# Kernel optimization log

Measured on AMD Instinct MI355X. Metric: run time of the kernel, lower is better.

The kernel has to match this reference:

```python
import jax, jax.numpy as jnp
import numpy as np

B, C, N = 8, 256, 2048

def setup_inputs() -> dict:
    key = jax.random.key(0)
    ks = jax.random.split(key, 7)
    s = 1.0 / np.sqrt(C)
    return {
        "x": jax.random.normal(ks[0], (B, C, N), dtype=jnp.float32),
        "Wq": jax.random.normal(ks[1], (C, C), dtype=jnp.float32) * s,
        "bq": jax.random.normal(ks[2], (C,), dtype=jnp.float32) * s,
        "Wk": jax.random.normal(ks[3], (C, C), dtype=jnp.float32) * s,
        "bk": jax.random.normal(ks[4], (C,), dtype=jnp.float32) * s,
        "Wv": jax.random.normal(ks[5], (C, C), dtype=jnp.float32) * s,
        "bv": jax.random.normal(ks[6], (C,), dtype=jnp.float32) * s,
    }

def reference(x, Wq, bq, Wk, bk, Wv, bv):
    # x: [B, C, N]; Conv1d(k=1) == channel-mixing matmul + bias
    q = jnp.einsum('oc,bcn->bon', Wq, x) + bq[None, :, None]  # [B,C,N]
    k = jnp.einsum('oc,bcn->bon', Wk, x) + bk[None, :, None]  # [B,C,N]
    v = jnp.einsum('oc,bcn->bon', Wv, x) + bv[None, :, None]  # [B,C,N]
    # qk = bmm(q^T, k): [B, N, N]
    qk = jnp.einsum('bcn,bcm->bnm', q, k)
    # global-sum normalization over the ENTIRE qk tensor (not row-wise softmax)
    attn_w = qk / jnp.sum(qk)
    # attn = bmm(v, attn_w): [B, C, N]
    attn = jnp.einsum('bcn,bnm->bcm', v, attn_w)
    return attn
```

## Files before the change

### kernel.cpp

```cpp
#include <hip/hip_runtime.h>


typedef _Float16 half8 __attribute__((ext_vector_type(8)));
typedef _Float16 half4 __attribute__((ext_vector_type(4)));
typedef _Float16 half2v __attribute__((ext_vector_type(2)));
typedef float f4v __attribute__((ext_vector_type(4)));

#define GP  40
#define GPB 36

__launch_bounds__(256)
__global__ void k1_kernel(const float* __restrict__ x, const float* __restrict__ Wq,
                          const float* __restrict__ Wk, const float* __restrict__ bq,
                          const float* __restrict__ bk, float* __restrict__ sxpart,
                          float* __restrict__ W3, float* __restrict__ u2,
                          float* __restrict__ w1, float* __restrict__ s1,
                          float* __restrict__ S, float* __restrict__ Gpart) {
    __shared__ __align__(16) char smem[40960];
    const int blk = blockIdx.x, t = threadIdx.x;
    if (blk < 192) {
        _Float16* Ah = (_Float16*)smem;
        _Float16* Al = Ah + 128 * GP;
        _Float16* Bh = Al + 128 * GP;
        _Float16* Bl = Bh + 128 * GP;
        const int tileId = blk >> 6;
        const int y = blk & 63;
        const int b = y >> 3, ks = y & 7;
        const int r0 = (tileId == 2) ? 128 : 0;
        const int c0 = (tileId == 0) ? 0 : 128;
        const bool diag = (tileId != 1);
        const float* xb = x + (long)b * 524288;

        const int lane = t & 63, wave = t >> 6;
        const int wy = wave >> 1, wx = wave & 1;
        const int mIn = lane & 15, quad = lane >> 4;

        f4v acc[4][4] = {};
        const int aBase = (wy * 64 + mIn) * GP + quad * 8;
        const int bBase = (wx * 64 + mIn) * GP + quad * 8;
        const int srow = t >> 3;
        const int skq  = (t & 7) * 4;
        float rs[4] = {};

        float4 pa[4], pb[4];
        int kk = ks * 256;
        #pragma unroll
        for (int i = 0; i < 4; ++i) {
            pa[i] = *(const float4*)&xb[(long)(r0 + srow + i * 32) * 2048 + kk + skq];
            if (!diag) pb[i] = *(const float4*)&xb[(long)(c0 + srow + i * 32) * 2048 + kk + skq];
        }

        for (int kb = 0; kb < 8; ++kb) {
            if (kb) __syncthreads();
            #pragma unroll
            for (int i = 0; i < 4; ++i) {
                const int row = srow + i * 32;
                half4 hv, lv;
                hv[0] = (_Float16)pa[i].x; lv[0] = (_Float16)(pa[i].x - (float)hv[0]);
                hv[1] = (_Float16)pa[i].y; lv[1] = (_Float16)(pa[i].y - (float)hv[1]);
                hv[2] = (_Float16)pa[i].z; lv[2] = (_Float16)(pa[i].z - (float)hv[2]);
                hv[3] = (_Float16)pa[i].w; lv[3] = (_Float16)(pa[i].w - (float)hv[3]);
                *(half4*)&Ah[row * GP + skq] = hv;
                *(half4*)&Al[row * GP + skq] = lv;
                if (diag) {
                    rs[i] += pa[i].x + pa[i].y + pa[i].z + pa[i].w;
                } else {
                    half4 hb, lb;
                    hb[0] = (_Float16)pb[i].x; lb[0] = (_Float16)(pb[i].x - (float)hb[0]);
                    hb[1] = (_Float16)pb[i].y; lb[1] = (_Float16)(pb[i].y - (float)hb[1]);
                    hb[2] = (_Float16)pb[i].z; lb[2] = (_Float16)(pb[i].z - (float)hb[2]);
                    hb[3] = (_Float16)pb[i].w; lb[3] = (_Float16)(pb[i].w - (float)hb[3]);
                    *(half4*)&Bh[row * GP + skq] = hb;
                    *(half4*)&Bl[row * GP + skq] = lb;
                }
            }
            __syncthreads();
            kk += 32;
            if (kb < 7) {
                #pragma unroll
                for (int i = 0; i < 4; ++i) {
                    pa[i] = *(const float4*)&xb[(long)(r0 + srow + i * 32) * 2048 + kk + skq];
                    if (!diag) pb[i] = *(const float4*)&xb[(long)(c0 + srow + i * 32) * 2048 + kk + skq];
                }
            }
            const _Float16* BhP = diag ? Ah : Bh;
            const _Float16* BlP = diag ? Al : Bl;
            #pragma unroll
            for (int ph = 0; ph < 3; ++ph) {
                const _Float16* As = (ph == 2) ? Al : Ah;
                const _Float16* Bs = (ph == 1) ? BlP : BhP;
                half8 af[4], bf[4];
                #pragma unroll
                for (int i = 0; i < 4; ++i) {
                    af[i] = *(const half8*)&As[aBase + i * 16 * GP];
                    bf[i] = *(const half8*)&Bs[bBase + i * 16 * GP];
                }
                #pragma unroll
                for (int i = 0; i < 4; ++i)
                    #pragma unroll
                    for (int j = 0; j < 4; ++j)
                        acc[i][j] = __builtin_amdgcn_mfma_f32_16x16x32_f16(af[i], bf[j], acc[i][j], 0, 0, 0);
            }
        }

        if (diag) {
            #pragma unroll
            for (int i = 0; i < 4; ++i) {
                rs[i] += __shfl_xor(rs[i], 1);
                rs[i] += __shfl_xor(rs[i], 2);
                rs[i] += __shfl_xor(rs[i], 4);
            }
            if ((t & 7) == 0) {
                #pragma unroll
                for (int i = 0; i < 4; ++i)
                    sxpart[ks * 2048 + b * 256 + r0 + srow + i * 32] = rs[i];
            }
        }

        float* D = Gpart + ((long)(ks * 8 + b) << 16);
        #pragma unroll
        for (int i = 0; i < 4; ++i)
            #pragma unroll
            for (int j = 0; j < 4; ++j) {
                const int row = r0 + wy * 64 + i * 16 + quad * 4;
                const int col = c0 + wx * 64 + j * 16 + mIn;
                #pragma unroll
                for (int r = 0; r < 4; ++r)
                    D[(row + r) * 256 + col] = acc[i][j][r];
                if (tileId == 1)
                    *(float4*)&D[(long)col * 256 + row] =
                        make_float4(acc[i][j][0], acc[i][j][1], acc[i][j][2], acc[i][j][3]);
            }
    } else if (blk < 208) {
        float* ldsA = (float*)smem;
        float* ldsB = ldsA + 16 * 68;
        const int tile = blk - 192;
        const int r0 = (tile >> 2) * 64, j0 = (tile & 3) * 64;
        const int tx = t & 15, ty = t >> 4;
        float acc[4][4] = {};
        for (int kk = 0; kk < 256; kk += 16) {
            *(float4*)&ldsA[ty * 68 + tx * 4] = *(const float4*)&Wq[(long)(kk + ty) * 256 + r0 + tx * 4];
            *(float4*)&ldsB[ty * 68 + tx * 4] = *(const float4*)&Wk[(long)(kk + ty) * 256 + j0 + tx * 4];
            __syncthreads();
            #pragma unroll
            for (int k = 0; k < 16; ++k) {
                const float4 av4 = *(const float4*)&ldsA[k * 68 + ty * 4];
                const float4 bv4 = *(const float4*)&ldsB[k * 68 + tx * 4];
                const float ar[4] = {av4.x, av4.y, av4.z, av4.w};
                const float br[4] = {bv4.x, bv4.y, bv4.z, bv4.w};
                #pragma unroll
                for (int i = 0; i < 4; ++i)
                    #pragma unroll
                    for (int j = 0; j < 4; ++j)
                        acc[i][j] = fmaf(ar[i], br[j], acc[i][j]);
            }
            __syncthreads();
        }
        #pragma unroll
        for (int i = 0; i < 4; ++i)
            *(float4*)&W3[(long)(r0 + ty * 4 + i) * 256 + j0 + tx * 4] =
                make_float4(acc[i][0], acc[i][1], acc[i][2], acc[i][3]);
    } else {
        float* sbq = (float*)smem;
        float* sbk = sbq + 256;
        float* red = sbk + 256;
        if (t == 0) S[0] = 0.0f;
        sbq[t] = bq[t]; sbk[t] = bk[t];
        __syncthreads();
        float u = 0.0f, w = 0.0f;
        #pragma unroll 8
        for (int c = 0; c < 256; ++c) {
            u = fmaf(Wk[(long)c * 256 + t], sbq[c], u);
            w = fmaf(Wq[(long)c * 256 + t], sbk[c], w);
        }
        u2[t] = u; w1[t] = w;
        red[t] = sbq[t] * sbk[t]; __syncthreads();
        for (int h = 128; h > 0; h >>= 1) { if (t < h) red[t] += red[t + h]; __syncthreads(); }
        if (t == 0) s1[0] = red[0];
    }
}

__launch_bounds__(256)
__global__ void k2_kernel(const float* __restrict__ Wv, const float* __restrict__ Gpart,
                          const float* __restrict__ W3, const float* __restrict__ u2,
                          const float* __restrict__ w1, const float* __restrict__ s1p,
                          const float* __restrict__ sxpart, float* __restrict__ T1,
                          float* __restrict__ v2, float* __restrict__ s2,
                          float* __restrict__ wvsx, float* __restrict__ S) {
    __shared__ __align__(16) char smem[40960];
    const int blk = blockIdx.x, t = threadIdx.x;
    if (blk < 128) {
        float* ldsA = (float*)smem;
        float* ldsB = ldsA + 16 * 68;
        const int r0 = (blk >> 5) * 64;
        const int g  = blk & 31;
        const int b  = g >> 2;
        const int j0 = (g & 3) * 64;
        const int tx = t & 15, ty = t >> 4;
        const int sr = t >> 2, sk = (t & 3) * 4;
        float acc[4][4] = {};
        for (int kk = 0; kk < 256; kk += 16) {
            const float4 a4 = *(const float4*)&Wv[(long)(r0 + sr) * 256 + kk + sk];
            ldsA[(sk + 0) * 68 + sr] = a4.x;
            ldsA[(sk + 1) * 68 + sr] = a4.y;
            ldsA[(sk + 2) * 68 + sr] = a4.z;
            ldsA[(sk + 3) * 68 + sr] = a4.w;
            float4 bs = make_float4(0.f, 0.f, 0.f, 0.f);
            #pragma unroll
            for (int ksl = 0; ksl < 8; ++ksl) {
                const float4 g4 = *(const float4*)&Gpart[(long)ksl * 524288 + (long)b * 65536 +
                                                         (long)(kk + ty) * 256 + j0 + tx * 4];
                bs.x += g4.x; bs.y += g4.y; bs.z += g4.z; bs.w += g4.w;
            }
            *(float4*)&ldsB[ty * 68 + tx * 4] = bs;
            __syncthreads();
            #pragma unroll
            for (int k = 0; k < 16; ++k) {
                const float4 av4 = *(const float4*)&ldsA[k * 68 + ty * 4];
                const float4 bv4 = *(const float4*)&ldsB[k * 68 + tx * 4];
                const float ar[4] = {av4.x, av4.y, av4.z, av4.w};
                const float br[4] = {bv4.x, bv4.y, bv4.z, bv4.w};
                #pragma unroll
                for (int i = 0; i < 4; ++i)
                    #pragma unroll
                    for (int j = 0; j < 4; ++j)
                        acc[i][j] = fmaf(ar[i], br[j], acc[i][j]);
            }
            __syncthreads();
        }
        float* D = T1 + (long)b * 65536;
        #pragma unroll
        for (int i = 0; i < 4; ++i)
            *(float4*)&D[(long)(r0 + ty * 4 + i) * 256 + j0 + tx * 4] =
                make_float4(acc[i][0], acc[i][1], acc[i][2], acc[i][3]);
    } else if (blk < 136) {
        float* ssx = (float*)smem;
        float* red = ssx + 256;
        const int b = blk - 128, j = t;
        float sxv = 0.0f;
        #pragma unroll
        for (int ks = 0; ks < 8; ++ks) sxv += sxpart[ks * 2048 + b * 256 + j];
        ssx[j] = sxv;
        __syncthreads();
        float vr = 0.0f;
        #pragma unroll 8
        for (int c = 0; c < 256; ++c) vr = fmaf(W3[(long)c * 256 + j], ssx[c], vr);
        const float v2j = vr + 2048.0f * u2[j];
        v2[b * 256 + j] = v2j;
        red[j] = v2j * sxv; __syncthreads();
        for (int h = 128; h > 0; h >>= 1) { if (j < h) red[j] += red[j + h]; __syncthreads(); }
        const float sd1 = red[0];
        __syncthreads();
        red[j] = sxv * w1[j]; __syncthreads();
        for (int h = 128; h > 0; h >>= 1) { if (j < h) red[j] += red[j + h]; __syncthreads(); }
        if (j == 0) {
            const float s2v = red[0] + 2048.0f * s1p[0];
            s2[b] = s2v;
            atomicAdd(S, sd1 + 2048.0f * s2v);
        }
    } else {
        float* wtile = (float*)smem;
        float* sxs = wtile + 8192;
        const int r0w = (blk - 136) * 32;
        #pragma unroll
        for (int p = 0; p < 8; ++p) {
            const int f = t + p * 256;
            const int row = f >> 6, c4 = f & 63;
            *(float4*)&wtile[row * 256 + c4 * 4] = *(const float4*)&Wv[(long)(r0w + row) * 256 + c4 * 4];
        }
        #pragma unroll
        for (int p = 0; p < 8; ++p) {
            const int f = t + p * 256;
            float s = 0.0f;
            #pragma unroll
            for (int ks = 0; ks < 8; ++ks) s += sxpart[ks * 2048 + f];
            sxs[f] = s;
        }
        __syncthreads();
        const int r = t >> 3, q = t & 7;
        float acc[8] = {};
        for (int ci = 0; ci < 32; ++ci) {
            const float wv = wtile[r * 256 + q * 32 + ci];
            #pragma unroll
            for (int b = 0; b < 8; ++b) acc[b] = fmaf(wv, sxs[b * 256 + q * 32 + ci], acc[b]);
        }
        #pragma unroll
        for (int b = 0; b < 8; ++b) {
            acc[b] += __shfl_xor(acc[b], 1);
            acc[b] += __shfl_xor(acc[b], 2);
            acc[b] += __shfl_xor(acc[b], 4);
        }
        if (q == 0) {
            #pragma unroll
            for (int b = 0; b < 8; ++b) wvsx[b * 256 + r0w + r] = acc[b];
        }
    }
}

__launch_bounds__(256)
__global__ void ap_kernel(const float* __restrict__ T1, const float* __restrict__ W3,
                          const float* __restrict__ wvsx, const float* __restrict__ u2,
                          const float* __restrict__ bv, const float* __restrict__ v2,
                          const float* __restrict__ w1, const float* __restrict__ s1p,
                          const float* __restrict__ s2, _Float16* __restrict__ Aph,
                          _Float16* __restrict__ Apl, float* __restrict__ cvec) {
    __shared__ float ldsA[16 * 68], ldsB[16 * 68], sw1[256];
    const int b = blockIdx.z;
    const int r0 = blockIdx.y * 64, j0 = blockIdx.x * 64;
    const float* A = T1 + (long)b * 65536;
    const int t = threadIdx.x, tx = t & 15, ty = t >> 4;
    const int sr = t >> 2, sk = (t & 3) * 4;
    sw1[t] = w1[t];
    float acc[4][4] = {};
    float dot[4] = {};
    for (int kk = 0; kk < 256; kk += 16) {
        const float4 a4 = *(const float4*)&A[(long)(r0 + sr) * 256 + kk + sk];
        ldsA[(sk + 0) * 68 + sr] = a4.x;
        ldsA[(sk + 1) * 68 + sr] = a4.y;
        ldsA[(sk + 2) * 68 + sr] = a4.z;
        ldsA[(sk + 3) * 68 + sr] = a4.w;
        *(float4*)&ldsB[ty * 68 + tx * 4] = *(const float4*)&W3[(long)(kk + ty) * 256 + j0 + tx * 4];
        __syncthreads();
        #pragma unroll
        for (int k = 0; k < 16; ++k) {
            const float4 av4 = *(const float4*)&ldsA[k * 68 + ty * 4];
            const float4 bv4 = *(const float4*)&ldsB[k * 68 + tx * 4];
            const float ar[4] = {av4.x, av4.y, av4.z, av4.w};
            const float br[4] = {bv4.x, bv4.y, bv4.z, bv4.w};
            const float wk = sw1[kk + k];
            #pragma unroll
            for (int i = 0; i < 4; ++i) {
                dot[i] = fmaf(ar[i], wk, dot[i]);
                #pragma unroll
                for (int j = 0; j < 4; ++j)
                    acc[i][j] = fmaf(ar[i], br[j], acc[i][j]);
            }
        }
        __syncthreads();
    }
    #pragma unroll
    for (int i = 0; i < 4; ++i) {
        const int r = r0 + ty * 4 + i;
        const float e1 = wvsx[b * 256 + r], e3 = bv[r];
        half4 hv, lv;
        #pragma unroll
        for (int j = 0; j < 4; ++j) {
            const int col = j0 + tx * 4 + j;
            const float val = acc[i][j] + e1 * u2[col] + e3 * v2[b * 256 + col];
            hv[j] = (_Float16)val;
            lv[j] = (_Float16)(val - (float)hv[j]);
        }
        const long o = (long)b * 65536 + (long)r * 256 + j0 + tx * 4;
        *(half4*)&Aph[o] = hv;
        *(half4*)&Apl[o] = lv;
        if (j0 == 0 && tx == 0)
            cvec[b * 256 + r] = dot[i] + e1 * s1p[0] + e3 * s2[b];
    }
}

__launch_bounds__(256)
__global__ void gemmF_mfma(const _Float16* __restrict__ Aph, const _Float16* __restrict__ Apl,
                           const float* __restrict__ x, const float* __restrict__ Sptr,
                           const float* __restrict__ cvec, float* __restrict__ out) {
    __shared__ __align__(16) _Float16 Ah[128 * GP];
    __shared__ __align__(16) _Float16 Al[128 * GP];
    __shared__ __align__(16) _Float16 Bh[128 * GPB];
    __shared__ __align__(16) _Float16 Bl[128 * GPB];
    __shared__ __align__(16) float xt[32 * 132];

    const int n0 = blockIdx.x * 128;
    const int c0 = blockIdx.y * 128;
    const int b = blockIdx.z;
    const _Float16* Asrc_h = Aph + (long)b * 65536;
    const _Float16* Asrc_l = Apl + (long)b * 65536;
    const float* xb = x + (long)b * 524288;

    const int t = threadIdx.x;
    const int lane = t & 63, wave = t >> 6;
    const int wy = wave >> 1, wx = wave & 1;
    const int mIn = lane & 15, quad = lane >> 4;

    f4v acc[4][4] = {};
    const int aBase = (wy * 64 + mIn) * GP + quad * 8;
    const int bBase = (wx * 64 + mIn) * GPB + quad * 8;
    const int cn = t & 127;
    const int ckh = (t >> 7) * 16;

    for (int kk = 0; kk < 256; kk += 32) {
        #pragma unroll
        for (int i = 0; i < 2; ++i) {
            const int idx = t + (i << 8);
            const int row = idx >> 2, ko = (idx & 3) << 3;
            *(uint4*)&Ah[row * GP + ko] = *(const uint4*)&Asrc_h[(long)(c0 + row) * 256 + kk + ko];
            *(uint4*)&Al[row * GP + ko] = *(const uint4*)&Asrc_l[(long)(c0 + row) * 256 + kk + ko];
        }
        #pragma unroll
        for (int p = 0; p < 4; ++p) {
            const int f = t + p * 256;
            const int k = f >> 5, n4 = f & 31;
            *(float4*)&xt[k * 132 + n4 * 4] = *(const float4*)&xb[(long)(kk + k) * 2048 + n0 + n4 * 4];
        }
        __syncthreads();
        {
            _Float16 hs[16], ls[16];
            #pragma unroll
            for (int k = 0; k < 16; ++k) {
                const float v = xt[(ckh + k) * 132 + cn];
                hs[k] = (_Float16)v;
                ls[k] = (_Float16)(v - (float)hs[k]);
            }
            #pragma unroll
            for (int k2 = 0; k2 < 8; ++k2) {
                half2v h2; h2[0] = hs[2 * k2]; h2[1] = hs[2 * k2 + 1];
                half2v l2; l2[0] = ls[2 * k2]; l2[1] = ls[2 * k2 + 1];
                *(half2v*)&Bh[cn * GPB + ckh + 2 * k2] = h2;
                *(half2v*)&Bl[cn * GPB + ckh + 2 * k2] = l2;
            }
        }
        __syncthreads();
        #pragma unroll
        for (int ph = 0; ph < 3; ++ph) {
            const _Float16* As = (ph == 2) ? Al : Ah;
            const _Float16* Bs = (ph == 1) ? Bl : Bh;
            half8 af[4], bf[4];
            #pragma unroll
            for (int i = 0; i < 4; ++i) {
                af[i] = *(const half8*)&As[aBase + i * 16 * GP];
                const half4 b0 = *(const half4*)&Bs[bBase + i * 16 * GPB];
                const half4 b1 = *(const half4*)&Bs[bBase + i * 16 * GPB + 4];
                bf[i] = __builtin_shufflevector(b0, b1, 0, 1, 2, 3, 4, 5, 6, 7);
            }
            #pragma unroll
            for (int i = 0; i < 4; ++i)
                #pragma unroll
                for (int j = 0; j < 4; ++j)
                    acc[i][j] = __builtin_amdgcn_mfma_f32_16x16x32_f16(af[i], bf[j], acc[i][j], 0, 0, 0);
        }
        __syncthreads();
    }

    const float invS = 1.0f / Sptr[0];
    float* ob = out + (long)b * 524288;
    const float* cv = cvec + b * 256;
    #pragma unroll
    for (int i = 0; i < 4; ++i)
        #pragma unroll
        for (int r = 0; r < 4; ++r) {
            const int row = c0 + wy * 64 + i * 16 + quad * 4 + r;
            const float c = cv[row];
            #pragma unroll
            for (int j = 0; j < 4; ++j) {
                const int col = n0 + wx * 64 + j * 16 + mIn;
                ob[(long)row * 2048 + col] = (acc[i][j][r] + c) * invS;
            }
        }
}

extern "C" void kernel_launch(void* const* d_in, const int* in_sizes, int n_in,
                              void* d_out, int out_size, void* d_ws, size_t ws_size,
                              hipStream_t stream) {
    const float* x  = (const float*)d_in[0];
    const float* Wq = (const float*)d_in[1];
    const float* bq = (const float*)d_in[2];
    const float* Wk = (const float*)d_in[3];
    const float* bk = (const float*)d_in[4];
    const float* Wv = (const float*)d_in[5];
    const float* bv = (const float*)d_in[6];
    float* out = (float*)d_out;
    float* ws  = (float*)d_ws;

    float* T1     = ws;
    float* W3     = ws + 524288;
    float* sxpart = ws + 589824;
    float* wvsx   = ws + 606208;
    float* v2     = ws + 608256;
    float* cvec   = ws + 610304;
    float* s2     = ws + 612352;
    float* u2     = ws + 612360;
    float* w1     = ws + 612616;
    float* s1     = ws + 612872;
    float* S      = ws + 612873;
    float* Gpart  = ws + 612880;
    _Float16* Aph = (_Float16*)(ws + 4807184);
    _Float16* Apl = Aph + 524288;

    k1_kernel<<<dim3(209), 256, 0, stream>>>(x, Wq, Wk, bq, bk, sxpart, W3, u2, w1, s1, S, Gpart);
    k2_kernel<<<dim3(144), 256, 0, stream>>>(Wv, Gpart, W3, u2, w1, s1, sxpart, T1, v2, s2, wvsx, S);
    ap_kernel<<<dim3(4, 4, 8), 256, 0, stream>>>(T1, W3, wvsx, u2, bv, v2, w1, s1, s2, Aph, Apl, cvec);
    gemmF_mfma<<<dim3(16, 2, 8), 256, 0, stream>>>(Aph, Apl, x, S, cvec, out);
}
```

Baseline: 152.8 us.

## Halve GEMM tile rows and add register prefetch across k2, ap and gemmF kernels

The small fp32 GEMMs in k2 and ap now use 32x64 tiles with a 32-deep k step, which doubles block count (k2 GEMM part 128 to 256 blocks, ap grid y 4 to 8) for more occupancy on the many CUs. All three kernels (k2, ap, gemmF_mfma) now prefetch the next k-slice of global data into registers while the current LDS tile is consumed. The goal is to hide global load latency and raise parallelism. The cost is higher register pressure and duplicated loads of the B operand across the extra row tiles.

```diff
diff --git a/kernel.cpp b/kernel.cpp
--- a/kernel.cpp
+++ b/kernel.cpp
@@ -189,54 +189,73 @@
                           float* __restrict__ wvsx, float* __restrict__ S) {
     __shared__ __align__(16) char smem[40960];
     const int blk = blockIdx.x, t = threadIdx.x;
-    if (blk < 128) {
+    if (blk < 256) {
         float* ldsA = (float*)smem;
-        float* ldsB = ldsA + 16 * 68;
-        const int r0 = (blk >> 5) * 64;
+        float* ldsB = ldsA + 32 * 34;
+        const int r0 = (blk >> 5) * 32;
         const int g  = blk & 31;
         const int b  = g >> 2;
         const int j0 = (g & 3) * 64;
         const int tx = t & 15, ty = t >> 4;
-        const int sr = t >> 2, sk = (t & 3) * 4;
-        float acc[4][4] = {};
-        for (int kk = 0; kk < 256; kk += 16) {
-            const float4 a4 = *(const float4*)&Wv[(long)(r0 + sr) * 256 + kk + sk];
-            ldsA[(sk + 0) * 68 + sr] = a4.x;
-            ldsA[(sk + 1) * 68 + sr] = a4.y;
-            ldsA[(sk + 2) * 68 + sr] = a4.z;
-            ldsA[(sk + 3) * 68 + sr] = a4.w;
-            float4 bs = make_float4(0.f, 0.f, 0.f, 0.f);
-            #pragma unroll
-            for (int ksl = 0; ksl < 8; ++ksl) {
-                const float4 g4 = *(const float4*)&Gpart[(long)ksl * 524288 + (long)b * 65536 +
-                                                         (long)(kk + ty) * 256 + j0 + tx * 4];
-                bs.x += g4.x; bs.y += g4.y; bs.z += g4.z; bs.w += g4.w;
-            }
-            *(float4*)&ldsB[ty * 68 + tx * 4] = bs;
+        const int ar = t >> 3, ak4 = (t & 7) * 4;
+        const float* Gb = Gpart + (long)b * 65536 + j0;
+        float acc[2][4] = {};
+
+        f4v pa, pg[2][8];
+        pa = *(const f4v*)&Wv[(long)(r0 + ar) * 256 + ak4];
+        #pragma unroll
+        for (int s = 0; s < 2; ++s)
+            #pragma unroll
+            for (int ksl = 0; ksl < 8; ++ksl)
+                pg[s][ksl] = *(const f4v*)&Gb[(long)ksl * 524288 + (long)(s * 16 + ty) * 256 + tx * 4];
+
+        for (int c = 0; c < 8; ++c) {
+            const int kk = c * 32;
+            ldsA[(ak4 + 0) * 34 + ar] = pa[0];
+            ldsA[(ak4 + 1) * 34 + ar] = pa[1];
+            ldsA[(ak4 + 2) * 34 + ar] = pa[2];
+            ldsA[(ak4 + 3) * 34 + ar] = pa[3];
+            #pragma unroll
+            for (int s = 0; s < 2; ++s) {
+                f4v bs = pg[s][0];
+                #pragma unroll
+                for (int ksl = 1; ksl < 8; ++ksl) bs += pg[s][ksl];
+                *(f4v*)&ldsB[(s * 16 + ty) * 68 + tx * 4] = bs;
+            }
             __syncthreads();
-            #pragma unroll
-            for (int k = 0; k < 16; ++k) {
-                const float4 av4 = *(const float4*)&ldsA[k * 68 + ty * 4];
+            if (c < 7) {
+                const int kn = kk + 32;
+                pa = *(const f4v*)&Wv[(long)(r0 + ar) * 256 + kn + ak4];
+                #pragma unroll
+                for (int s = 0; s < 2; ++s)
+                    #pragma unroll
+                    for (int ksl = 0; ksl < 8; ++ksl)
+                        pg[s][ksl] = *(const f4v*)&Gb[(long)ksl * 524288 + (long)(kn + s * 16 + ty) * 256 + tx * 4];
+            }
+            #pragma unroll
+            for (int k = 0; k < 32; ++k) {
+                const float2 av2 = *(const float2*)&ldsA[k * 34 + ty * 2];
                 const float4 bv4 = *(const float4*)&ldsB[k * 68 + tx * 4];
-                const float ar[4] = {av4.x, av4.y, av4.z, av4.w};
-                const float br[4] = {bv4.x, bv4.y, bv4.z, bv4.w};
-                #pragma unroll
-                for (int i = 0; i < 4; ++i)
-                    #pragma unroll
-                    for (int j = 0; j < 4; ++j)
-                        acc[i][j] = fmaf(ar[i], br[j], acc[i][j]);
+                acc[0][0] = fmaf(av2.x, bv4.x, acc[0][0]);
+                acc[0][1] = fmaf(av2.x, bv4.y, acc[0][1]);
+                acc[0][2] = fmaf(av2.x, bv4.z, acc[0][2]);
+                acc[0][3] = fmaf(av2.x, bv4.w, acc[0][3]);
+                acc[1][0] = fmaf(av2.y, bv4.x, acc[1][0]);
+                acc[1][1] = fmaf(av2.y, bv4.y, acc[1][1]);
+                acc[1][2] = fmaf(av2.y, bv4.z, acc[1][2]);
+                acc[1][3] = fmaf(av2.y, bv4.w, acc[1][3]);
             }
             __syncthreads();
         }
         float* D = T1 + (long)b * 65536;
         #pragma unroll
-        for (int i = 0; i < 4; ++i)
-            *(float4*)&D[(long)(r0 + ty * 4 + i) * 256 + j0 + tx * 4] =
+        for (int i = 0; i < 2; ++i)
+            *(float4*)&D[(long)(r0 + ty * 2 + i) * 256 + j0 + tx * 4] =
                 make_float4(acc[i][0], acc[i][1], acc[i][2], acc[i][3]);
-    } else if (blk < 136) {
+    } else if (blk < 264) {
         float* ssx = (float*)smem;
         float* red = ssx + 256;
-        const int b = blk - 128, j = t;
+        const int b = blk - 256, j = t;
         float sxv = 0.0f;
         #pragma unroll
         for (int ks = 0; ks < 8; ++ks) sxv += sxpart[ks * 2048 + b * 256 + j];
@@ -261,7 +280,7 @@
     } else {
         float* wtile = (float*)smem;
         float* sxs = wtile + 8192;
-        const int r0w = (blk - 136) * 32;
+        const int r0w = (blk - 264) * 32;
         #pragma unroll
         for (int p = 0; p < 8; ++p) {
             const int f = t + p * 256;
@@ -304,43 +323,59 @@
                           const float* __restrict__ w1, const float* __restrict__ s1p,
                           const float* __restrict__ s2, _Float16* __restrict__ Aph,
                           _Float16* __restrict__ Apl, float* __restrict__ cvec) {
-    __shared__ float ldsA[16 * 68], ldsB[16 * 68], sw1[256];
+    __shared__ __align__(16) float ldsA[32 * 34];
+    __shared__ __align__(16) float ldsB[32 * 68];
+    __shared__ float sw1[256];
     const int b = blockIdx.z;
-    const int r0 = blockIdx.y * 64, j0 = blockIdx.x * 64;
+    const int r0 = blockIdx.y * 32, j0 = blockIdx.x * 64;
     const float* A = T1 + (long)b * 65536;
     const int t = threadIdx.x, tx = t & 15, ty = t >> 4;
-    const int sr = t >> 2, sk = (t & 3) * 4;
+    const int ar = t >> 3, ak4 = (t & 7) * 4;
     sw1[t] = w1[t];
-    float acc[4][4] = {};
-    float dot[4] = {};
-    for (int kk = 0; kk < 256; kk += 16) {
-        const float4 a4 = *(const float4*)&A[(long)(r0 + sr) * 256 + kk + sk];
-        ldsA[(sk + 0) * 68 + sr] = a4.x;
-        ldsA[(sk + 1) * 68 + sr] = a4.y;
-        ldsA[(sk + 2) * 68 + sr] = a4.z;
-        ldsA[(sk + 3) * 68 + sr] = a4.w;
-        *(float4*)&ldsB[ty * 68 + tx * 4] = *(const float4*)&W3[(long)(kk + ty) * 256 + j0 + tx * 4];
-        __syncthreads();
-        #pragma unroll
-        for (int k = 0; k < 16; ++k) {
-            const float4 av4 = *(const float4*)&ldsA[k * 68 + ty * 4];
+    float acc[2][4] = {};
+    float dot[2] = {};
+
+    f4v pa, pb[2];
+    pa = *(const f4v*)&A[(long)(r0 + ar) * 256 + ak4];
+    pb[0] = *(const f4v*)&W3[(long)(ty) * 256 + j0 + tx * 4];
+    pb[1] = *(const f4v*)&W3[(long)(16 + ty) * 256 + j0 + tx * 4];
+
+    for (int c = 0; c < 8; ++c) {
+        const int kk = c * 32;
+        ldsA[(ak4 + 0) * 34 + ar] = pa[0];
+        ldsA[(ak4 + 1) * 34 + ar] = pa[1];
+        ldsA[(ak4 + 2) * 34 + ar] = pa[2];
+        ldsA[(ak4 + 3) * 34 + ar] = pa[3];
+        *(f4v*)&ldsB[ty * 68 + tx * 4] = pb[0];
+        *(f4v*)&ldsB[(16 + ty) * 68 + tx * 4] = pb[1];
+        __syncthreads();
+        if (c < 7) {
+            const int kn = kk + 32;
+            pa = *(const f4v*)&A[(long)(r0 + ar) * 256 + kn + ak4];
+            pb[0] = *(const f4v*)&W3[(long)(kn + ty) * 256 + j0 + tx * 4];
+            pb[1] = *(const f4v*)&W3[(long)(kn + 16 + ty) * 256 + j0 + tx * 4];
+        }
+        #pragma unroll
+        for (int k = 0; k < 32; ++k) {
+            const float2 av2 = *(const float2*)&ldsA[k * 34 + ty * 2];
             const float4 bv4 = *(const float4*)&ldsB[k * 68 + tx * 4];
-            const float ar[4] = {av4.x, av4.y, av4.z, av4.w};
-            const float br[4] = {bv4.x, bv4.y, bv4.z, bv4.w};
             const float wk = sw1[kk + k];
-            #pragma unroll
-            for (int i = 0; i < 4; ++i) {
-                dot[i] = fmaf(ar[i], wk, dot[i]);
-                #pragma unroll
-                for (int j = 0; j < 4; ++j)
-                    acc[i][j] = fmaf(ar[i], br[j], acc[i][j]);
-            }
+            dot[0] = fmaf(av2.x, wk, dot[0]);
+            dot[1] = fmaf(av2.y, wk, dot[1]);
+            acc[0][0] = fmaf(av2.x, bv4.x, acc[0][0]);
+            acc[0][1] = fmaf(av2.x, bv4.y, acc[0][1]);
+            acc[0][2] = fmaf(av2.x, bv4.z, acc[0][2]);
+            acc[0][3] = fmaf(av2.x, bv4.w, acc[0][3]);
+            acc[1][0] = fmaf(av2.y, bv4.x, acc[1][0]);
+            acc[1][1] = fmaf(av2.y, bv4.y, acc[1][1]);
+            acc[1][2] = fmaf(av2.y, bv4.z, acc[1][2]);
+            acc[1][3] = fmaf(av2.y, bv4.w, acc[1][3]);
         }
         __syncthreads();
     }
     #pragma unroll
-    for (int i = 0; i < 4; ++i) {
-        const int r = r0 + ty * 4 + i;
+    for (int i = 0; i < 2; ++i) {
+        const int r = r0 + ty * 2 + i;
         const float e1 = wvsx[b * 256 + r], e3 = bv[r];
         half4 hv, lv;
         #pragma unroll
@@ -386,20 +421,31 @@
     const int cn = t & 127;
     const int ckh = (t >> 7) * 16;
 
+    int arow[2], ako[2], xk[4], xn[4];
+    #pragma unroll
+    for (int i = 0; i < 2; ++i) { const int idx = t + (i << 8); arow[i] = idx >> 2; ako[i] = (idx & 3) << 3; }
+    #pragma unroll
+    for (int p = 0; p < 4; ++p) { const int f = t + p * 256; xk[p] = f >> 5; xn[p] = f & 31; }
+
+    uint4 pah[2], pal[2]; f4v px[4];
+    #pragma unroll
+    for (int i = 0; i < 2; ++i) {
+        pah[i] = *(const uint4*)&Asrc_h[(long)(c0 + arow[i]) * 256 + ako[i]];
+        pal[i] = *(const uint4*)&Asrc_l[(long)(c0 + arow[i]) * 256 + ako[i]];
+    }
+    #pragma unroll
+    for (int p = 0; p < 4; ++p)
+        px[p] = *(const f4v*)&xb[(long)xk[p] * 2048 + n0 + xn[p] * 4];
+
     for (int kk = 0; kk < 256; kk += 32) {
         #pragma unroll
         for (int i = 0; i < 2; ++i) {
-            const int idx = t + (i << 8);
-            const int row = idx >> 2, ko = (idx & 3) << 3;
-            *(uint4*)&Ah[row * GP + ko] = *(const uint4*)&Asrc_h[(long)(c0 + row) * 256 + kk + ko];
-            *(uint4*)&Al[row * GP + ko] = *(const uint4*)&Asrc_l[(long)(c0 + row) * 256 + kk + ko];
-        }
-        #pragma unroll
-        for (int p = 0; p < 4; ++p) {
-            const int f = t + p * 256;
-            const int k = f >> 5, n4 = f & 31;
-            *(float4*)&xt[k * 132 + n4 * 4] = *(const float4*)&xb[(long)(kk + k) * 2048 + n0 + n4 * 4];
-        }
+            *(uint4*)&Ah[arow[i] * GP + ako[i]] = pah[i];
+            *(uint4*)&Al[arow[i] * GP + ako[i]] = pal[i];
+        }
+        #pragma unroll
+        for (int p = 0; p < 4; ++p)
+            *(f4v*)&xt[xk[p] * 132 + xn[p] * 4] = px[p];
         __syncthreads();
         {
             _Float16 hs[16], ls[16];
@@ -418,6 +464,17 @@
             }
         }
         __syncthreads();
+        if (kk < 224) {
+            const int kn = kk + 32;
+            #pragma unroll
+            for (int i = 0; i < 2; ++i) {
+                pah[i] = *(const uint4*)&Asrc_h[(long)(c0 + arow[i]) * 256 + kn + ako[i]];
+                pal[i] = *(const uint4*)&Asrc_l[(long)(c0 + arow[i]) * 256 + kn + ako[i]];
+            }
+            #pragma unroll
+            for (int p = 0; p < 4; ++p)
+                px[p] = *(const f4v*)&xb[(long)(kn + xk[p]) * 2048 + n0 + xn[p] * 4];
+        }
         #pragma unroll
         for (int ph = 0; ph < 3; ++ph) {
             const _Float16* As = (ph == 2) ? Al : Ah;
@@ -485,7 +542,7 @@
     _Float16* Apl = Aph + 524288;
 
     k1_kernel<<<dim3(209), 256, 0, stream>>>(x, Wq, Wk, bq, bk, sxpart, W3, u2, w1, s1, S, Gpart);
-    k2_kernel<<<dim3(144), 256, 0, stream>>>(Wv, Gpart, W3, u2, w1, s1, sxpart, T1, v2, s2, wvsx, S);
-    ap_kernel<<<dim3(4, 4, 8), 256, 0, stream>>>(T1, W3, wvsx, u2, bv, v2, w1, s1, s2, Aph, Apl, cvec);
+    k2_kernel<<<dim3(272), 256, 0, stream>>>(Wv, Gpart, W3, u2, w1, s1, sxpart, T1, v2, s2, wvsx, S);
+    ap_kernel<<<dim3(4, 8, 8), 256, 0, stream>>>(T1, W3, wvsx, u2, bv, v2, w1, s1, s2, Aph, Apl, cvec);
     gemmF_mfma<<<dim3(16, 2, 8), 256, 0, stream>>>(Aph, Apl, x, S, cvec, out);
 }
```

New measurement: 154.3 us. About the same (+1.0%).
